# Performance work log

Measured on AMD Instinct MI355X. Metric: run time of the kernel, lower is better.

Reference implementation:

```python
import jax, jax.numpy as jnp
import numpy as np

N_NODES = 50000
N_EDGES = 800000
D = 64  # in_feat == hidden_channels


def _param(key, shape, fan_in):
    return jax.random.normal(key, shape, dtype=jnp.float32) / np.sqrt(fan_in)


def setup_inputs() -> dict:
    key = jax.random.key(0)
    ks = jax.random.split(key, 32)
    inp = {
        "x": jax.random.normal(ks[0], (N_NODES, D), dtype=jnp.float32),
        "edge_index": jax.random.randint(ks[1], (2, N_EDGES), 0, N_NODES, dtype=jnp.int64),
    }
    i = 2
    for l in (1, 2, 3):
        inp[f"W1_{l}"] = _param(ks[i + 0], (D, D), D)   # LEConv lin1 (source nodes)
        inp[f"b1_{l}"] = jnp.zeros((D,), jnp.float32)
        inp[f"W2_{l}"] = _param(ks[i + 1], (D, D), D)   # LEConv lin2 (target nodes, no bias)
        inp[f"W3_{l}"] = _param(ks[i + 2], (D, D), D)   # LEConv lin3 (root/self)
        inp[f"b3_{l}"] = jnp.zeros((D,), jnp.float32)
        inp[f"Wl_{l}"] = _param(ks[i + 3], (D, D), D)   # post-conv Linear
        inp[f"bl_{l}"] = jnp.zeros((D,), jnp.float32)
        i += 4
    return inp


def _leconv(x, src, dst, W1, b1, W2, W3, b3):
    # out_i = lin3(x_i) + sum_{j->i} (lin1(x_j) - lin2(x_i))
    a = x @ W1 + b1          # [N, D]
    b = x @ W2               # [N, D]
    msg = a[src] - b[dst]    # [E, D]  gather + elementwise
    agg = jax.ops.segment_sum(msg, dst, num_segments=x.shape[0])  # scatter-add
    return agg + (x @ W3 + b3)


def reference(x, edge_index,
              W1_1, b1_1, W2_1, W3_1, b3_1, Wl_1, bl_1,
              W1_2, b1_2, W2_2, W3_2, b3_2, Wl_2, bl_2,
              W1_3, b1_3, W2_3, W3_3, b3_3, Wl_3, bl_3):
    src, dst = edge_index[0], edge_index[1]
    h = x
    for (W1, b1, W2, W3, b3, Wl, bl) in (
        (W1_1, b1_1, W2_1, W3_1, b3_1, Wl_1, bl_1),
        (W1_2, b1_2, W2_2, W3_2, b3_2, Wl_2, bl_2),
        (W1_3, b1_3, W2_3, W3_3, b3_3, Wl_3, bl_3),
    ):
        h = _leconv(h, src, dst, W1, b1, W2, W3, b3)
        h = jax.nn.relu(h @ Wl + bl)
    return h
```

## Files before the change

kernel.cpp:

```cpp
#include <hip/hip_runtime.h>

#define N_NODES 50000
#define N_EDGES 800000
#define NCHUNK 64
#define NRANGE 4
#define RNODES (N_NODES / NRANGE)
#define CEDGES (N_EDGES / NCHUNK)
#define HIST_NB (NCHUNK * NRANGE)
#define SCAN_NB2 ((N_NODES + 63) / 64)

typedef __attribute__((ext_vector_type(8))) short short8;
typedef __attribute__((ext_vector_type(4))) float f32x4;

struct LPtrs { const float *W1, *W2, *W3, *Wl, *b1, *b3, *bl; };
struct AllPtrs { LPtrs l[3]; };

__device__ inline unsigned short f2b(float f) {
    union { float f; unsigned u; } c; c.f = f;
    return (unsigned short)((c.u + 0x7FFFu + ((c.u >> 16) & 1u)) >> 16);
}
__device__ inline float b2f(unsigned short h) {
    union { unsigned u; float f; } c; c.u = ((unsigned)h) << 16;
    return c.f;
}

__global__ __launch_bounds__(256) void histpack_kernel(const int* __restrict__ dst,
                                                       unsigned char* __restrict__ hist_part,
                                                       AllPtrs ap,
                                                       unsigned short* __restrict__ Wp,
                                                       float* __restrict__ rows) {
    __shared__ unsigned int h[5248];
    const int t = threadIdx.x;
    if (blockIdx.x < HIST_NB) {
        const int chunk = blockIdx.x >> 2;
        const int range = blockIdx.x & 3;
        const int nbase = range * RNODES;
        for (int i = t; i < RNODES / 4; i += 256) h[i] = 0u;
        __syncthreads();
        const int* dp = dst + chunk * CEDGES;
        for (int i = t; i < CEDGES; i += 256) {
            int d = dp[i] - nbase;
            if ((unsigned)d < (unsigned)RNODES)
                atomicAdd(&h[d >> 2], 1u << ((d & 3) * 8));
        }
        __syncthreads();
        unsigned int* out = (unsigned int*)(hist_part + (long)chunk * N_NODES + nbase);
        for (int i = t; i < RNODES / 4; i += 256) out[i] = h[i];
    } else {
        float* sW = (float*)h;
        float* sL = (float*)h + 64 * 65;
        const int wi = blockIdx.x - HIST_NB;
        const int layer = wi / 12;
        const int ct = wi % 12;
        LPtrs L = ap.l[layer];
        const float* Wm = (ct < 4) ? L.W1 : (ct < 8) ? L.W2 : L.W3;
        const int colb = (ct & 3) * 16;
        for (int i = t; i < 64 * 64; i += 256) sW[(i >> 6) * 65 + (i & 63)] = Wm[i];
        for (int i = t; i < 64 * 16; i += 256) {
            int q = i >> 4, c = i & 15;
            sL[q * 17 + c] = L.Wl[q * 64 + colb + c];
        }
        __syncthreads();
        for (int local = t; local < 1024; local += 256) {
            int j = local & 7, lane = (local >> 3) & 63, s = local >> 9;
            int k = s * 32 + (lane >> 4) * 8 + j;
            int c = lane & 15;
            float acc = 0.f;
            #pragma unroll 8
            for (int q = 0; q < 64; ++q) acc += sW[k * 65 + q] * sL[q * 17 + c];
            Wp[layer * 12288 + ct * 1024 + local] = f2b(acc);
        }
        if (ct == 0 && t < 64) {
            int col = t;
            float r1 = 0.f, r3 = 0.f;
            for (int q = 0; q < 64; ++q) {
                float wl = L.Wl[q * 64 + col];
                r1 += L.b1[q] * wl;
                r3 += L.b3[q] * wl;
            }
            rows[layer * 128 + col] = r1;
            rows[layer * 128 + 64 + col] = r3 + L.bl[col];
        }
    }
}

__global__ __launch_bounds__(256) void scanA2_kernel(unsigned char* __restrict__ hist_part,
                                                     int* __restrict__ off,
                                                     int* __restrict__ deg,
                                                     int* __restrict__ bsum) {
    __shared__ int part[4][64];
    const int t = threadIdx.x;
    const int ln = t & 63;
    const int cg = t >> 6;
    const int node = blockIdx.x * 64 + ln;
    unsigned char* col = hist_part + node;
    unsigned char v[16];
    int s = 0;
    if (node < N_NODES) {
        #pragma unroll
        for (int k = 0; k < 16; ++k) {
            v[k] = col[(long)(cg * 16 + k) * N_NODES];
            s += v[k];
        }
    }
    part[cg][ln] = s;
    __syncthreads();
    int run = 0, tot = 0;
    #pragma unroll
    for (int g = 0; g < 4; ++g) {
        int p = part[g][ln];
        if (g < cg) run += p;
        tot += p;
    }
    if (node < N_NODES) {
        #pragma unroll
        for (int k = 0; k < 16; ++k) {
            col[(long)(cg * 16 + k) * N_NODES] = (unsigned char)run;
            run += v[k];
        }
        if (cg == 0) deg[node] = tot;
    }
    if (cg == 0) {
        int x = tot;
        #pragma unroll
        for (int d = 1; d < 64; d <<= 1) {
            int u = __shfl_up(x, d, 64);
            if (ln >= d) x += u;
        }
        if (node < N_NODES) off[node] = x - tot;
        if (ln == 63) bsum[blockIdx.x] = x;
    }
}

__device__ __forceinline__ void gemm_body(int blk, int t,
    const unsigned short* __restrict__ hbf, const float* __restrict__ hf32,
    const unsigned short* __restrict__ Wp,
    const int* __restrict__ deg, const float* __restrict__ rows,
    unsigned short* __restrict__ abf, unsigned short* __restrict__ wbf, int n)
{
    const int lane = t & 63;
    const int quad = lane >> 4, lm = lane & 15;
    const int row_base = blk * 64 + (t >> 6) * 16;

    int arow = min(row_base + lm, n - 1);
    short8 a0, a1;
    if (hf32) {
        const float* hrow = hf32 + (long)arow * 64;
        #pragma unroll
        for (int j = 0; j < 8; ++j) {
            a0[j] = (short)f2b(hrow[quad * 8 + j]);
            a1[j] = (short)f2b(hrow[32 + quad * 8 + j]);
        }
    } else {
        const unsigned short* hrow = hbf + (long)arow * 64;
        a0 = *(const short8*)(hrow + quad * 8);
        a1 = *(const short8*)(hrow + 32 + quad * 8);
    }

    const short8* wp = (const short8*)Wp;
    f32x4 acc[12];
    #pragma unroll
    for (int ct = 0; ct < 12; ++ct) {
        f32x4 z = {0.f, 0.f, 0.f, 0.f};
        short8 w0 = wp[(ct * 2 + 0) * 64 + lane];
        short8 w1 = wp[(ct * 2 + 1) * 64 + lane];
        z = __builtin_amdgcn_mfma_f32_16x16x32_bf16(a0, w0, z, 0, 0, 0);
        z = __builtin_amdgcn_mfma_f32_16x16x32_bf16(a1, w1, z, 0, 0, 0);
        acc[ct] = z;
    }

    const int g0 = row_base + quad * 4;
    float dg[4];
    #pragma unroll
    for (int r = 0; r < 4; ++r) dg[r] = (float)deg[min(g0 + r, n - 1)];

    #pragma unroll
    for (int ct = 0; ct < 4; ++ct) {
        int col = ct * 16 + lm;
        float r1 = rows[col];
        float r3 = rows[64 + col];
        #pragma unroll
        for (int r = 0; r < 4; ++r) {
            int g = g0 + r;
            if (g < n) {
                abf[(long)g * 64 + col] = f2b(acc[ct][r]);
                float wv = acc[8 + ct][r] - dg[r] * (acc[4 + ct][r] - r1) + r3;
                wbf[(long)g * 64 + col] = f2b(wv);
            }
        }
    }
}

__global__ __launch_bounds__(256) void gemm3w_kernel(
    const unsigned short* __restrict__ hbf, const float* __restrict__ hf32,
    const unsigned short* __restrict__ Wp,
    const int* __restrict__ deg, const float* __restrict__ rows,
    unsigned short* __restrict__ abf, unsigned short* __restrict__ wbf, int n)
{
    gemm_body(blockIdx.x, threadIdx.x, hbf, hf32, Wp, deg, rows, abf, wbf, n);
}

__global__ __launch_bounds__(256) void fillgemm_kernel(
    const int* __restrict__ src, const int* __restrict__ dst,
    const int* __restrict__ off, const int* __restrict__ bsum,
    int* __restrict__ boff, const unsigned char* __restrict__ hist_part,
    int* __restrict__ csr,
    const float* __restrict__ x, const unsigned short* __restrict__ Wp,
    const int* __restrict__ deg, const float* __restrict__ rows,
    unsigned short* __restrict__ abf, unsigned short* __restrict__ wbf)
{
    __shared__ int cur[RNODES];
    __shared__ int sb[SCAN_NB2 + 2];
    if (blockIdx.x >= HIST_NB) {
        gemm_body(blockIdx.x - HIST_NB, threadIdx.x, nullptr, x, Wp, deg, rows,
                  abf, wbf, N_NODES);
        return;
    }
    const int t = threadIdx.x;

    int carry = 0;
    for (int base = 0; base < SCAN_NB2; base += 256) {
        int idx = base + t;
        int v = (idx < SCAN_NB2) ? bsum[idx] : 0;
        cur[t] = v;
        __syncthreads();
        #pragma unroll
        for (int d = 1; d < 256; d <<= 1) {
            int u = (t >= d) ? cur[t - d] : 0;
            __syncthreads();
            cur[t] += u;
            __syncthreads();
        }
        if (idx < SCAN_NB2) sb[idx] = carry + cur[t] - v;
        carry += cur[255];
        __syncthreads();
    }
    if (blockIdx.x == 0)
        for (int i = t; i < SCAN_NB2; i += 256) boff[i] = sb[i];

    const int chunk = blockIdx.x >> 2;
    const int range = blockIdx.x & 3;
    const int nbase = range * RNODES;
    const unsigned char* bp = hist_part + (long)chunk * N_NODES + nbase;
    const int* op = off + nbase;
    for (int i = t; i < RNODES; i += 256)
        cur[i] = op[i] + sb[(nbase + i) >> 6] + (int)bp[i];
    __syncthreads();
    const int* dp = dst + chunk * CEDGES;
    const int* sp = src + chunk * CEDGES;
    for (int i = t; i < CEDGES; i += 256) {
        int d = dp[i] - nbase;
        if ((unsigned)d < (unsigned)RNODES) {
            int pos = atomicAdd(&cur[d], 1);
            csr[pos] = sp[i];
        }
    }
}

__global__ __launch_bounds__(256) void gather_out_kernel(
    const int* __restrict__ off, const int* __restrict__ boff,
    const int* __restrict__ degv, const int* __restrict__ csr,
    const unsigned short* __restrict__ abf,
    const unsigned short* __restrict__ wbf,
    float* __restrict__ out_f, unsigned short* __restrict__ out_b, int last)
{
    int node = blockIdx.x * 4 + (threadIdx.x >> 6);
    int lane = threadIdx.x & 63;
    const int g = lane >> 4;
    const int f = (lane & 15) * 4;
    int beg = off[node] + boff[node >> 6];
    int end = beg + degv[node];
    float ax = 0.f, ay = 0.f, az = 0.f, aw = 0.f;
    int j = beg;
    for (; j + 16 <= end; j += 16) {
        int s0 = csr[j + g], s1 = csr[j + 4 + g];
        int s2 = csr[j + 8 + g], s3 = csr[j + 12 + g];
        ushort4 v0 = *(const ushort4*)(abf + (long)s0 * 64 + f);
        ushort4 v1 = *(const ushort4*)(abf + (long)s1 * 64 + f);
        ushort4 v2 = *(const ushort4*)(abf + (long)s2 * 64 + f);
        ushort4 v3 = *(const ushort4*)(abf + (long)s3 * 64 + f);
        ax += b2f(v0.x) + b2f(v1.x) + b2f(v2.x) + b2f(v3.x);
        ay += b2f(v0.y) + b2f(v1.y) + b2f(v2.y) + b2f(v3.y);
        az += b2f(v0.z) + b2f(v1.z) + b2f(v2.z) + b2f(v3.z);
        aw += b2f(v0.w) + b2f(v1.w) + b2f(v2.w) + b2f(v3.w);
    }
    for (; j + 8 <= end; j += 8) {
        int s0 = csr[j + g], s1 = csr[j + 4 + g];
        ushort4 v0 = *(const ushort4*)(abf + (long)s0 * 64 + f);
        ushort4 v1 = *(const ushort4*)(abf + (long)s1 * 64 + f);
        ax += b2f(v0.x) + b2f(v1.x);
        ay += b2f(v0.y) + b2f(v1.y);
        az += b2f(v0.z) + b2f(v1.z);
        aw += b2f(v0.w) + b2f(v1.w);
    }
    for (; j < end; j += 4) {
        int jj = j + g;
        if (jj < end) {
            int s0 = csr[jj];
            ushort4 v0 = *(const ushort4*)(abf + (long)s0 * 64 + f);
            ax += b2f(v0.x); ay += b2f(v0.y); az += b2f(v0.z); aw += b2f(v0.w);
        }
    }
    #pragma unroll
    for (int m = 16; m < 64; m <<= 1) {
        ax += __shfl_xor(ax, m, 64);
        ay += __shfl_xor(ay, m, 64);
        az += __shfl_xor(az, m, 64);
        aw += __shfl_xor(aw, m, 64);
    }
    if (g == 0) {
        ushort4 wv = *(const ushort4*)(wbf + (long)node * 64 + f);
        float o0 = fmaxf(ax + b2f(wv.x), 0.f);
        float o1 = fmaxf(ay + b2f(wv.y), 0.f);
        float o2 = fmaxf(az + b2f(wv.z), 0.f);
        float o3 = fmaxf(aw + b2f(wv.w), 0.f);
        if (last) {
            float4 o = {o0, o1, o2, o3};
            *(float4*)(out_f + (long)node * 64 + f) = o;
        } else {
            ushort4 o;
            o.x = f2b(o0); o.y = f2b(o1); o.z = f2b(o2); o.w = f2b(o3);
            *(ushort4*)(out_b + (long)node * 64 + f) = o;
        }
    }
}

extern "C" void kernel_launch(void* const* d_in, const int* in_sizes, int n_in,
                              void* d_out, int out_size, void* d_ws, size_t ws_size,
                              hipStream_t stream) {
    const float* x  = (const float*)d_in[0];
    const int*   ei = (const int*)d_in[1];
    const int*   src = ei;
    const int*   dst = ei + N_EDGES;

    char* wsb = (char*)d_ws;
    unsigned char*  hist_part = (unsigned char*)(wsb);
    unsigned short* abf  = (unsigned short*)(wsb + 12800000);
    unsigned short* wbf  = (unsigned short*)(wsb + 19200000);
    unsigned short* h1   = (unsigned short*)(wsb + 25600000);
    unsigned short* Wp   = (unsigned short*)(wsb + 38400000);
    float*          rows = (float*)(wsb + 38500000);
    int* off  = (int*)(wsb + 38600000);
    int* deg  = off + N_NODES;
    int* bsum = deg + N_NODES;
    int* boff = bsum + 1024;
    int* csr  = boff + 1024;

    const int NBLK = (N_NODES + 63) / 64;

    AllPtrs ap;
    for (int l = 0; l < 3; ++l) {
        int base = 2 + l * 7;
        ap.l[l].W1 = (const float*)d_in[base + 0];
        ap.l[l].b1 = (const float*)d_in[base + 1];
        ap.l[l].W2 = (const float*)d_in[base + 2];
        ap.l[l].W3 = (const float*)d_in[base + 3];
        ap.l[l].b3 = (const float*)d_in[base + 4];
        ap.l[l].Wl = (const float*)d_in[base + 5];
        ap.l[l].bl = (const float*)d_in[base + 6];
    }

    histpack_kernel<<<HIST_NB + 36, 256, 0, stream>>>(dst, hist_part, ap, Wp, rows);
    scanA2_kernel<<<SCAN_NB2, 256, 0, stream>>>(hist_part, off, deg, bsum);
    fillgemm_kernel<<<HIST_NB + NBLK, 256, 0, stream>>>(
        src, dst, off, bsum, boff, hist_part, csr,
        x, Wp, deg, rows, abf, wbf);

    gather_out_kernel<<<N_NODES / 4, 256, 0, stream>>>(
        off, boff, deg, csr, abf, wbf, (float*)d_out, h1, 0);

    const unsigned short* hin = h1;
    for (int l = 1; l < 3; ++l) {
        gemm3w_kernel<<<NBLK, 256, 0, stream>>>(
            hin, nullptr, Wp + l * 12288, deg, rows + l * 128,
            abf, wbf, N_NODES);
        gather_out_kernel<<<N_NODES / 4, 256, 0, stream>>>(
            off, boff, deg, csr, abf, wbf, (float*)d_out, h1, (l == 2));
        hin = h1;
    }
}
```

Before: 266.8 us.

## Double edge chunks, single-pass block scan, and packed row offset/degree for gather

Raises the edge-chunk count from 64 to 128, so the CSR fill phase runs twice as many blocks with half the edges each; the column scan now walks 32 histogram rows per thread group. The per-block bsum scan in the fill kernel becomes one pass with four elements per thread, replacing the looped 256-wide scan. The fill kernel also writes each node's final CSR start and degree as one int2, so the three gather launches load one packed value instead of off, boff and deg. The trade-off is more histogram traffic and more fill blocks that each repeat the scan.

```diff
diff --git a/kernel.cpp b/kernel.cpp
--- a/kernel.cpp
+++ b/kernel.cpp
@@ -2,12 +2,13 @@
 
 #define N_NODES 50000
 #define N_EDGES 800000
-#define NCHUNK 64
+#define NCHUNK 128
 #define NRANGE 4
 #define RNODES (N_NODES / NRANGE)
 #define CEDGES (N_EDGES / NCHUNK)
 #define HIST_NB (NCHUNK * NRANGE)
-#define SCAN_NB2 ((N_NODES + 63) / 64)
+#define SCAN_NB 782
+#define NBLK 782
 
 typedef __attribute__((ext_vector_type(8))) short short8;
 typedef __attribute__((ext_vector_type(4))) float f32x4;
@@ -94,12 +95,12 @@
     const int cg = t >> 6;
     const int node = blockIdx.x * 64 + ln;
     unsigned char* col = hist_part + node;
-    unsigned char v[16];
+    unsigned char v[32];
     int s = 0;
     if (node < N_NODES) {
         #pragma unroll
-        for (int k = 0; k < 16; ++k) {
-            v[k] = col[(long)(cg * 16 + k) * N_NODES];
+        for (int k = 0; k < 32; ++k) {
+            v[k] = col[(long)(cg * 32 + k) * N_NODES];
             s += v[k];
         }
     }
@@ -114,13 +115,13 @@
     }
     if (node < N_NODES) {
         #pragma unroll
-        for (int k = 0; k < 16; ++k) {
-            col[(long)(cg * 16 + k) * N_NODES] = (unsigned char)run;
+        for (int k = 0; k < 32; ++k) {
+            col[(long)(cg * 32 + k) * N_NODES] = (unsigned char)run;
             run += v[k];
         }
-        if (cg == 0) deg[node] = tot;
     }
     if (cg == 0) {
+        if (node < N_NODES) deg[node] = tot;
         int x = tot;
         #pragma unroll
         for (int d = 1; d < 64; d <<= 1) {
@@ -203,14 +204,14 @@
 __global__ __launch_bounds__(256) void fillgemm_kernel(
     const int* __restrict__ src, const int* __restrict__ dst,
     const int* __restrict__ off, const int* __restrict__ bsum,
-    int* __restrict__ boff, const unsigned char* __restrict__ hist_part,
-    int* __restrict__ csr,
+    const unsigned char* __restrict__ hist_part,
+    int* __restrict__ csr, int2* __restrict__ rowinfo,
     const float* __restrict__ x, const unsigned short* __restrict__ Wp,
     const int* __restrict__ deg, const float* __restrict__ rows,
     unsigned short* __restrict__ abf, unsigned short* __restrict__ wbf)
 {
     __shared__ int cur[RNODES];
-    __shared__ int sb[SCAN_NB2 + 2];
+    __shared__ int sb[1024];
     if (blockIdx.x >= HIST_NB) {
         gemm_body(blockIdx.x - HIST_NB, threadIdx.x, nullptr, x, Wp, deg, rows,
                   abf, wbf, N_NODES);
@@ -218,33 +219,39 @@
     }
     const int t = threadIdx.x;
 
-    int carry = 0;
-    for (int base = 0; base < SCAN_NB2; base += 256) {
-        int idx = base + t;
-        int v = (idx < SCAN_NB2) ? bsum[idx] : 0;
-        cur[t] = v;
-        __syncthreads();
-        #pragma unroll
-        for (int d = 1; d < 256; d <<= 1) {
-            int u = (t >= d) ? cur[t - d] : 0;
-            __syncthreads();
-            cur[t] += u;
-            __syncthreads();
-        }
-        if (idx < SCAN_NB2) sb[idx] = carry + cur[t] - v;
-        carry += cur[255];
-        __syncthreads();
-    }
-    if (blockIdx.x == 0)
-        for (int i = t; i < SCAN_NB2; i += 256) boff[i] = sb[i];
+    const int i0 = t * 4;
+    int a0 = (i0 + 0 < SCAN_NB) ? bsum[i0 + 0] : 0;
+    int a1 = (i0 + 1 < SCAN_NB) ? bsum[i0 + 1] : 0;
+    int a2 = (i0 + 2 < SCAN_NB) ? bsum[i0 + 2] : 0;
+    int a3 = (i0 + 3 < SCAN_NB) ? bsum[i0 + 3] : 0;
+    int s = a0 + a1 + a2 + a3;
+    cur[t] = s;
+    __syncthreads();
+    #pragma unroll
+    for (int d = 1; d < 256; d <<= 1) {
+        int u = (t >= d) ? cur[t - d] : 0;
+        __syncthreads();
+        cur[t] += u;
+        __syncthreads();
+    }
+    int excl = cur[t] - s;
+    sb[i0 + 0] = excl;
+    sb[i0 + 1] = excl + a0;
+    sb[i0 + 2] = excl + a0 + a1;
+    sb[i0 + 3] = excl + a0 + a1 + a2;
+    __syncthreads();
 
     const int chunk = blockIdx.x >> 2;
     const int range = blockIdx.x & 3;
     const int nbase = range * RNODES;
     const unsigned char* bp = hist_part + (long)chunk * N_NODES + nbase;
     const int* op = off + nbase;
-    for (int i = t; i < RNODES; i += 256)
-        cur[i] = op[i] + sb[(nbase + i) >> 6] + (int)bp[i];
+    for (int i = t; i < RNODES; i += 256) {
+        int c = op[i] + sb[(nbase + i) >> 6] + (int)bp[i];
+        cur[i] = c;
+        if (chunk == 0)
+            rowinfo[nbase + i] = make_int2(c, deg[nbase + i]);
+    }
     __syncthreads();
     const int* dp = dst + chunk * CEDGES;
     const int* sp = src + chunk * CEDGES;
@@ -258,8 +265,7 @@
 }
 
 __global__ __launch_bounds__(256) void gather_out_kernel(
-    const int* __restrict__ off, const int* __restrict__ boff,
-    const int* __restrict__ degv, const int* __restrict__ csr,
+    const int2* __restrict__ rowinfo, const int* __restrict__ csr,
     const unsigned short* __restrict__ abf,
     const unsigned short* __restrict__ wbf,
     float* __restrict__ out_f, unsigned short* __restrict__ out_b, int last)
@@ -268,8 +274,9 @@
     int lane = threadIdx.x & 63;
     const int g = lane >> 4;
     const int f = (lane & 15) * 4;
-    int beg = off[node] + boff[node >> 6];
-    int end = beg + degv[node];
+    int2 ri = rowinfo[node];
+    int beg = ri.x;
+    int end = beg + ri.y;
     float ax = 0.f, ay = 0.f, az = 0.f, aw = 0.f;
     int j = beg;
     for (; j + 16 <= end; j += 16) {
@@ -340,13 +347,11 @@
     unsigned short* h1   = (unsigned short*)(wsb + 25600000);
     unsigned short* Wp   = (unsigned short*)(wsb + 38400000);
     float*          rows = (float*)(wsb + 38500000);
-    int* off  = (int*)(wsb + 38600000);
-    int* deg  = off + N_NODES;
-    int* bsum = deg + N_NODES;
-    int* boff = bsum + 1024;
-    int* csr  = boff + 1024;
-
-    const int NBLK = (N_NODES + 63) / 64;
+    int*  off     = (int*)(wsb + 38600000);
+    int*  deg     = (int*)(wsb + 38900000);
+    int*  bsum    = (int*)(wsb + 39200000);
+    int2* rowinfo = (int2*)(wsb + 39300000);
+    int*  csr     = (int*)(wsb + 39800000);
 
     AllPtrs ap;
     for (int l = 0; l < 3; ++l) {
@@ -361,13 +366,13 @@
     }
 
     histpack_kernel<<<HIST_NB + 36, 256, 0, stream>>>(dst, hist_part, ap, Wp, rows);
-    scanA2_kernel<<<SCAN_NB2, 256, 0, stream>>>(hist_part, off, deg, bsum);
+    scanA2_kernel<<<SCAN_NB, 256, 0, stream>>>(hist_part, off, deg, bsum);
     fillgemm_kernel<<<HIST_NB + NBLK, 256, 0, stream>>>(
-        src, dst, off, bsum, boff, hist_part, csr,
+        src, dst, off, bsum, hist_part, csr, rowinfo,
         x, Wp, deg, rows, abf, wbf);
 
     gather_out_kernel<<<N_NODES / 4, 256, 0, stream>>>(
-        off, boff, deg, csr, abf, wbf, (float*)d_out, h1, 0);
+        rowinfo, csr, abf, wbf, (float*)d_out, h1, 0);
 
     const unsigned short* hin = h1;
     for (int l = 1; l < 3; ++l) {
@@ -375,7 +380,7 @@
             hin, nullptr, Wp + l * 12288, deg, rows + l * 128,
             abf, wbf, N_NODES);
         gather_out_kernel<<<N_NODES / 4, 256, 0, stream>>>(
-            off, boff, deg, csr, abf, wbf, (float*)d_out, h1, (l == 2));
+            rowinfo, csr, abf, wbf, (float*)d_out, h1, (l == 2));
         hin = h1;
     }
 }
```

Result: no change. 268.9 us (+0.8%).
